# Performance work log

Hardware: AMD Instinct MI355X
Metric: run time of the kernel (lower is better)

Reference implementation:

```python
import jax, jax.numpy as jnp
import numpy as np

T, N, D, E, O = 2, 4096, 1024, 8, 1024

def setup_inputs() -> dict:
    key = jax.random.key(0)
    k1, k2, k3 = jax.random.split(key, 3)
    x = jax.random.normal(k1, (T, N, D), dtype=jnp.float32)
    Wg = jax.random.normal(k2, (T, D, E), dtype=jnp.float32) * (1.0 / np.sqrt(D))
    We = jax.random.normal(k3, (E, D, O), dtype=jnp.float32) * (1.0 / np.sqrt(D))
    return {"x": x, "Wg": Wg, "We": We, "k": 2}


def reference(x, Wg, We, k):
    # Per-task gating logits: [T, N, E]
    logits = jnp.einsum('tnd,tde->tne', x, Wg)
    # Top-k mask per token (scatter 1.0 at top-k indices)
    _, topk_idx = jax.lax.top_k(logits, k)                      # [T, N, k]
    mask = jax.nn.one_hot(topk_idx, E, dtype=logits.dtype).sum(-2)  # [T, N, E]
    masked = mask * logits
    gates = masked / (masked.sum(-1, keepdims=True) + 1e-9)     # [T, N, E]
    # Dense expert outputs (each expert is Linear(D, O)): [T, N, E, O]
    eout = jnp.einsum('tnd,edo->tneo', x, We)
    # Weighted combine over selected experts
    out = jnp.einsum('tne,tneo->tno', gates, eout)              # [T, N, O]
    return out
```

## Files before the change

### kernel.cpp

```cpp
#include <hip/hip_runtime.h>
#include <hip/hip_bf16.h>
#include <stdint.h>

#define T_ 2
#define N_ 4096
#define D_ 1024
#define E_ 8
#define O_ 1024

#define BM 128
#define BN 128
#define BK 32

typedef __attribute__((ext_vector_type(8))) short short8;
typedef __attribute__((ext_vector_type(4))) float f32x4;

#define AS1 __attribute__((address_space(1)))
#define AS3 __attribute__((address_space(3)))

__device__ inline void gld16(const unsigned short* g, unsigned short* l) {
    __builtin_amdgcn_global_load_lds((const AS1 unsigned int*)g,
                                     (AS3 unsigned int*)l, 16, 0, 0);
}

__device__ inline unsigned short f2bf(float f) {
    union { float f; unsigned u; } v; v.f = f;
    unsigned r = v.u + 0x7fff + ((v.u >> 16) & 1);
    return (unsigned short)(r >> 16);
}

__global__ __launch_bounds__(256) void prep_kernel(
    const float* __restrict__ x, const float* __restrict__ Wg,
    const float* __restrict__ We,
    unsigned short* __restrict__ xb, unsigned short* __restrict__ Wbp,
    int* __restrict__ route, float2* __restrict__ gpair,
    float* __restrict__ out)
{
    __shared__ __align__(16) char smem[E_ * D_ * 4];
    int tid = threadIdx.x;

    if (blockIdx.x >= 2048) {
        float4 z = {0.f, 0.f, 0.f, 0.f};
        float4* dst = (float4*)out + (size_t)(blockIdx.x - 2048) * 1024;
#pragma unroll
        for (int k = 0; k < 4; ++k) dst[k * 256 + tid] = z;
        return;
    }

    if (blockIdx.x < 1024) {
        float (*WgT)[D_] = (float(*)[D_])smem;
        int wave = tid >> 6, lane = tid & 63;
        int token0 = blockIdx.x * 8;
        int t = token0 >> 12;
        const float* wgb = Wg + (size_t)t * D_ * E_;

#pragma unroll
        for (int r = 0; r < 8; ++r) {
            int f = r * 1024 + tid * 4;
            float4 v = *(const float4*)(wgb + f);
            WgT[f & 7][f >> 3]             = v.x;
            WgT[(f + 1) & 7][(f + 1) >> 3] = v.y;
            WgT[(f + 2) & 7][(f + 2) >> 3] = v.z;
            WgT[(f + 3) & 7][(f + 3) >> 3] = v.w;
        }
        __syncthreads();

#pragma unroll
        for (int tl = 0; tl < 2; ++tl) {
            int token = token0 + wave * 2 + tl;
            const float* xrow = x + (size_t)token * D_;

            float4 xv[4];
#pragma unroll
            for (int c = 0; c < 4; ++c)
                xv[c] = *(const float4*)(xrow + c * 256 + lane * 4);

            float acc[E_] = {0.f, 0.f, 0.f, 0.f, 0.f, 0.f, 0.f, 0.f};
#pragma unroll
            for (int c = 0; c < 4; ++c) {
                int d0 = c * 256 + lane * 4;
                unsigned lo = f2bf(xv[c].x) | ((unsigned)f2bf(xv[c].y) << 16);
                unsigned hi = f2bf(xv[c].z) | ((unsigned)f2bf(xv[c].w) << 16);
                *(uint2*)(&xb[(size_t)token * D_ + d0]) = make_uint2(lo, hi);
#pragma unroll
                for (int e = 0; e < E_; ++e) {
                    float4 w = *(const float4*)(&WgT[e][d0]);
                    acc[e] += xv[c].x * w.x + xv[c].y * w.y + xv[c].z * w.z + xv[c].w * w.w;
                }
            }
#pragma unroll
            for (int off = 1; off < 64; off <<= 1) {
#pragma unroll
                for (int e = 0; e < E_; ++e) acc[e] += __shfl_xor(acc[e], off, 64);
            }

            if (lane == 0) {
                float best = acc[0]; int bi = 0;
#pragma unroll
                for (int e = 1; e < E_; ++e) if (acc[e] > best) { best = acc[e]; bi = e; }
                float sec = -INFINITY; int si = 0;
#pragma unroll
                for (int e = 0; e < E_; ++e) if (e != bi && acc[e] > sec) { sec = acc[e]; si = e; }
                float s = best + sec + 1e-9f;
                route[token] = bi | (si << 8);
                gpair[token] = make_float2(best / s, sec / s);
            }
        }
    } else {
        unsigned short* P = (unsigned short*)smem;

        int b = blockIdx.x - 1024;
        int e  = b >> 7;
        int oy = (b & 127) >> 3;
        int dz = b & 7;
        int o0 = oy * 64, d0 = dz * 128;

#pragma unroll
        for (int r = 0; r < 32; ++r) {
            int lin = r * 256 + tid;
            int dd = lin >> 6, oo = lin & 63;
            P[oo * 136 + dd] = f2bf(We[((size_t)(e * D_ + d0 + dd)) * O_ + o0 + oo]);
        }
        __syncthreads();

#pragma unroll
        for (int w = 0; w < 4; ++w) {
            int ci   = w * 256 + tid;
            int lane = ci & 63;
            int c16  = (ci >> 6) & 3;
            int ks   = ci >> 8;
            int fr = lane & 15, q = lane >> 4;
            uint4 v = *(const uint4*)&P[(c16 * 16 + fr) * 136 + ks * 32 + q * 8];
            int ot  = oy >> 1;
            int cb  = (oy * 4 + c16) & 7;
            int ksa = dz * 4 + ks;
            size_t idx = ((((size_t)(e * 8 + ot) * 32 + ksa) * 8 + cb) * 64 + lane) * 8;
            *(uint4*)(Wbp + idx) = v;
        }
    }
}

__global__ __launch_bounds__(1024) void build_lists(
    const int* __restrict__ route, const float2* __restrict__ gpair,
    int* __restrict__ toklist, float* __restrict__ gatelist,
    int* __restrict__ counts)
{
    int g = blockIdx.x;
    int t = g >> 3, e = g & 7;
    int tid = threadIdx.x;
    int wave = tid >> 6, lane = tid & 63;

    __shared__ int waveSum[16];

    int4 r4 = *(const int4*)(route + t * N_ + tid * 4);
    int rr[4] = {r4.x, r4.y, r4.z, r4.w};
    int sel[4], slot[4], mycnt = 0;
#pragma unroll
    for (int j = 0; j < 4; ++j) {
        int e0 = rr[j] & 255, e1 = (rr[j] >> 8) & 255;
        sel[j]  = (e0 == e) || (e1 == e);
        slot[j] = (e0 == e) ? 0 : 1;
        mycnt  += sel[j];
    }
    int x = mycnt;
#pragma unroll
    for (int off = 1; off < 64; off <<= 1) {
        int y = __shfl_up(x, off, 64);
        if (lane >= off) x += y;
    }
    if (lane == 63) waveSum[wave] = x;
    __syncthreads();
    int woff = 0, total = 0;
#pragma unroll
    for (int w = 0; w < 16; ++w) {
        int s = waveSum[w];
        total += s;
        woff += (w < wave) ? s : 0;
    }
    int p = woff + x - mycnt;
#pragma unroll
    for (int j = 0; j < 4; ++j) {
        if (sel[j]) {
            int n = tid * 4 + j;
            toklist[g * N_ + p] = n | (slot[j] << 16);
            float2 gp = gpair[t * N_ + n];
            gatelist[g * N_ + p] = (slot[j] == 0) ? gp.x : gp.y;
            ++p;
        }
    }
    if (tid == 0) counts[g] = total;
}

__global__ __launch_bounds__(512, 4) void moe_gemm(
    const unsigned short* __restrict__ xb,
    const unsigned short* __restrict__ Wbp,
    const int* __restrict__ toklist, const float* __restrict__ gatelist,
    const int* __restrict__ counts, float* __restrict__ out)
{
    int lin = blockIdx.x;
    int mt  = lin >> 7;
    int u   = lin & 127;
    int xcd = u & 7;
    int v   = u >> 3;
    int g   = 2 * xcd + (v >> 3);
    int ot  = v & 7;
    int t   = g >> 3;

    int cnt = counts[g];
    int m0 = mt * BM;
    if (m0 >= cnt) return;

    __shared__ __align__(16) unsigned short As[2][BM * BK];
    __shared__ int   tokS[BM];
    __shared__ float gateS[BM];

    int tid = threadIdx.x;
    if (tid < BM) {
        int r = m0 + tid;
        tokS[tid]  = (r < cnt) ? toklist[g * N_ + r]  : -1;
        gateS[tid] = (r < cnt) ? gatelist[g * N_ + r] : 0.f;
    }
    __syncthreads();

    int wave = tid >> 6, lane = tid & 63;
    int lr = lane >> 2;
    int sg = (lane & 3) ^ ((lane >> 3) & 3);
    int ar = wave * 16 + lr;
    int tok = max(tokS[ar], 0) & 0xFFFF;
    const unsigned short* ag = xb + ((size_t)(t * N_ + tok)) * D_ + sg * 8;

    const unsigned short* wf =
        Wbp + ((size_t)((g & 7) * 8 + ot) * 32) * 4096;
    int cb0 = (wave >> 1) * 2;
    const unsigned short* bp0 = wf + cb0 * 512 + lane * 8;
    const unsigned short* bp1 = bp0 + 512;

    int fr = lane & 15, q = lane >> 4;
    int wm = (wave & 1) * 64;
    int wn = (wave >> 1) * 32;
    int fp = (q ^ ((fr >> 1) & 3)) * 8;

    f32x4 acc[4][2];
#pragma unroll
    for (int mi = 0; mi < 4; ++mi)
#pragma unroll
        for (int ni = 0; ni < 2; ++ni) acc[mi][ni] = (f32x4){0.f, 0.f, 0.f, 0.f};

    short8 bf0[2], bf1[2];

    gld16(ag, &As[0][wave * 512]);
    asm volatile("" ::: "memory");
    bf0[0] = *(const short8*)(bp0);
    bf0[1] = *(const short8*)(bp1);

#define KSTEP(CUR, NXT, BC, BNX, IT)                                           \
    {                                                                          \
        asm volatile("s_waitcnt vmcnt(2)" ::: "memory");     \
        __builtin_amdgcn_s_barrier();                                          \
        asm volatile("" ::: "memory");       \
        int kk = (IT) + 1;                                                     \
        if (kk < D_ / BK) {                                                    \
            gld16(ag + (size_t)kk * BK, &As[NXT][wave * 512]);                 \
            asm volatile("" ::: "memory");     \
            BNX[0] = *(const short8*)(bp0 + (size_t)kk * 4096);                \
            BNX[1] = *(const short8*)(bp1 + (size_t)kk * 4096);                \
        }                                                                      \
        short8 af[4];                                                          \
        _Pragma("unroll") for (int mi = 0; mi < 4; ++mi)                       \
            af[mi] = *(const short8*)(&As[CUR][(wm + mi * 16 + fr) * BK + fp]);\
        _Pragma("unroll") for (int mi = 0; mi < 4; ++mi) {                     \
            acc[mi][0] = __builtin_amdgcn_mfma_f32_16x16x32_bf16(              \
                af[mi], BC[0], acc[mi][0], 0, 0, 0);                           \
            acc[mi][1] = __builtin_amdgcn_mfma_f32_16x16x32_bf16(              \
                af[mi], BC[1], acc[mi][1], 0, 0, 0);                           \
        }                                                                      \
    }

    for (int it = 0; it < D_ / BK; it += 2) {
        KSTEP(0, 1, bf0, bf1, it)
        KSTEP(1, 0, bf1, bf0, it + 1)
    }
#undef KSTEP

    float* outb = out + (size_t)t * N_ * O_;
    int ncol = ot * 128 + wn + fr;
#pragma unroll
    for (int mi = 0; mi < 4; ++mi) {
#pragma unroll
        for (int r = 0; r < 4; ++r) {
            int ml = wm + mi * 16 + q * 4 + r;
            int ent = tokS[ml];
            if (ent >= 0) {
                int tokk = ent & 0xFFFF;
                float gate = gateS[ml];
                float* orow = outb + (size_t)tokk * O_ + ncol;
#pragma unroll
                for (int ni = 0; ni < 2; ++ni)
                    unsafeAtomicAdd(orow + ni * 16, gate * acc[mi][ni][r]);
            }
        }
    }
}

extern "C" void kernel_launch(void* const* d_in, const int* in_sizes, int n_in,
                              void* d_out, int out_size, void* d_ws, size_t ws_size,
                              hipStream_t stream)
{
    const float* x  = (const float*)d_in[0];
    const float* Wg = (const float*)d_in[1];
    const float* We = (const float*)d_in[2];
    float* out = (float*)d_out;

    char* ws = (char*)d_ws;
    unsigned short* xb   = (unsigned short*)(ws);
    unsigned short* Wbp  = (unsigned short*)(ws + 16777216);
    int*   toklist       = (int*)  (ws + 33554432);
    float* gatelist      = (float*)(ws + 33816576);
    int*   counts        = (int*)  (ws + 34078720);
    int*   route         = (int*)  (ws + 34078976);
    float2* gpair        = (float2*)(ws + 34111744);

    prep_kernel<<<4096, 256, 0, stream>>>(x, Wg, We, xb, Wbp, route, gpair, out);
    build_lists<<<T_ * E_, 1024, 0, stream>>>(route, gpair, toklist, gatelist, counts);
    moe_gemm<<<(N_ / BM) * 8 * (T_ * E_), 512, 0, stream>>>(
        xb, Wbp, toklist, gatelist, counts, out);
}
```

Measured before the change: 198.3 us.

## Replace atomic output accumulation with per-slot bf16 stores and a combine pass

Drops the zero-fill of the fp32 output and the float atomics. Each GEMM tile now stores its gated result as bf16 into one half of the fp32 output word, picked by the token's top-k slot, and a new combine kernel adds the two halves. The prep kernel also gives each gate block twice as many tokens and switches the weight repack to float4 loads over smaller tiles, and the GEMM tile order is permuted. This saves the memset and atomic traffic but adds a full read and write pass over the output and rounds each expert's contribution to bf16, which costs accuracy.

```diff
diff --git a/kernel.cpp b/kernel.cpp
--- a/kernel.cpp
+++ b/kernel.cpp
@@ -33,24 +33,15 @@
     const float* __restrict__ x, const float* __restrict__ Wg,
     const float* __restrict__ We,
     unsigned short* __restrict__ xb, unsigned short* __restrict__ Wbp,
-    int* __restrict__ route, float2* __restrict__ gpair,
-    float* __restrict__ out)
+    int* __restrict__ route, float2* __restrict__ gpair)
 {
     __shared__ __align__(16) char smem[E_ * D_ * 4];
     int tid = threadIdx.x;
 
-    if (blockIdx.x >= 2048) {
-        float4 z = {0.f, 0.f, 0.f, 0.f};
-        float4* dst = (float4*)out + (size_t)(blockIdx.x - 2048) * 1024;
-#pragma unroll
-        for (int k = 0; k < 4; ++k) dst[k * 256 + tid] = z;
-        return;
-    }
-
-    if (blockIdx.x < 1024) {
+    if (blockIdx.x < 512) {
         float (*WgT)[D_] = (float(*)[D_])smem;
         int wave = tid >> 6, lane = tid & 63;
-        int token0 = blockIdx.x * 8;
+        int token0 = blockIdx.x * 16;
         int t = token0 >> 12;
         const float* wgb = Wg + (size_t)t * D_ * E_;
 
@@ -66,8 +57,8 @@
         __syncthreads();
 
 #pragma unroll
-        for (int tl = 0; tl < 2; ++tl) {
-            int token = token0 + wave * 2 + tl;
+        for (int tl = 0; tl < 4; ++tl) {
+            int token = token0 + wave * 4 + tl;
             const float* xrow = x + (size_t)token * D_;
 
             float4 xv[4];
@@ -109,32 +100,35 @@
     } else {
         unsigned short* P = (unsigned short*)smem;
 
-        int b = blockIdx.x - 1024;
+        int b  = blockIdx.x - 512;
         int e  = b >> 7;
-        int oy = (b & 127) >> 3;
-        int dz = b & 7;
-        int o0 = oy * 64, d0 = dz * 128;
-
-#pragma unroll
-        for (int r = 0; r < 32; ++r) {
-            int lin = r * 256 + tid;
-            int dd = lin >> 6, oo = lin & 63;
-            P[oo * 136 + dd] = f2bf(We[((size_t)(e * D_ + d0 + dd)) * O_ + o0 + oo]);
+        int r7 = b & 127;
+        int dz = r7 >> 2;
+        int ob = r7 & 3;
+        int d0 = dz * 32, o0 = ob * 256;
+
+#pragma unroll
+        for (int it = 0; it < 8; ++it) {
+            int lin = it * 256 + tid;
+            int dd = lin >> 6, o4 = lin & 63;
+            float4 v = *(const float4*)(We + ((size_t)(e * D_ + d0 + dd)) * O_ + o0 + o4 * 4);
+            P[(o4 * 4 + 0) * 40 + dd] = f2bf(v.x);
+            P[(o4 * 4 + 1) * 40 + dd] = f2bf(v.y);
+            P[(o4 * 4 + 2) * 40 + dd] = f2bf(v.z);
+            P[(o4 * 4 + 3) * 40 + dd] = f2bf(v.w);
         }
         __syncthreads();
 
 #pragma unroll
-        for (int w = 0; w < 4; ++w) {
-            int ci   = w * 256 + tid;
+        for (int it = 0; it < 4; ++it) {
+            int ci   = it * 256 + tid;
+            int cbl  = ci >> 6;
             int lane = ci & 63;
-            int c16  = (ci >> 6) & 3;
-            int ks   = ci >> 8;
             int fr = lane & 15, q = lane >> 4;
-            uint4 v = *(const uint4*)&P[(c16 * 16 + fr) * 136 + ks * 32 + q * 8];
-            int ot  = oy >> 1;
-            int cb  = (oy * 4 + c16) & 7;
-            int ksa = dz * 4 + ks;
-            size_t idx = ((((size_t)(e * 8 + ot) * 32 + ksa) * 8 + cb) * 64 + lane) * 8;
+            uint4 v = *(const uint4*)&P[(cbl * 16 + fr) * 40 + q * 8];
+            int ot = ob * 2 + (cbl >> 3);
+            int cb = cbl & 7;
+            size_t idx = ((((size_t)(e * 8 + ot) * 32 + dz) * 8 + cb) * 64 + lane) * 8;
             *(uint4*)(Wbp + idx) = v;
         }
     }
@@ -198,7 +192,8 @@
     const int* __restrict__ counts, float* __restrict__ out)
 {
     int lin = blockIdx.x;
-    int mt  = lin >> 7;
+    int qm  = lin >> 7;
+    int mt  = (qm == 0) ? 8 : (qm <= 8 ? qm - 1 : qm);
     int u   = lin & 127;
     int xcd = u & 7;
     int v   = u >> 3;
@@ -292,14 +287,30 @@
             int ent = tokS[ml];
             if (ent >= 0) {
                 int tokk = ent & 0xFFFF;
+                int slot = ent >> 16;
                 float gate = gateS[ml];
-                float* orow = outb + (size_t)tokk * O_ + ncol;
-#pragma unroll
-                for (int ni = 0; ni < 2; ++ni)
-                    unsafeAtomicAdd(orow + ni * 16, gate * acc[mi][ni][r]);
+#pragma unroll
+                for (int ni = 0; ni < 2; ++ni) {
+                    unsigned short* p =
+                        (unsigned short*)(outb + (size_t)tokk * O_ + ncol + ni * 16);
+                    p[slot] = f2bf(gate * acc[mi][ni][r]);
+                }
             }
         }
     }
+}
+
+__global__ __launch_bounds__(256) void combine_kernel(float* __restrict__ out)
+{
+    size_t i = ((size_t)blockIdx.x * 256 + threadIdx.x) * 4;
+    unsigned* po = (unsigned*)out;
+    uint4 v = *(uint4*)(po + i);
+    float4 r;
+    union { unsigned u; float f; } a, b;
+#define CMB(comp, src) a.u = (src) << 16; b.u = (src) & 0xFFFF0000u; comp = a.f + b.f
+    CMB(r.x, v.x); CMB(r.y, v.y); CMB(r.z, v.z); CMB(r.w, v.w);
+#undef CMB
+    *(float4*)(out + i) = r;
 }
 
 extern "C" void kernel_launch(void* const* d_in, const int* in_sizes, int n_in,
@@ -320,8 +331,9 @@
     int*   route         = (int*)  (ws + 34078976);
     float2* gpair        = (float2*)(ws + 34111744);
 
-    prep_kernel<<<4096, 256, 0, stream>>>(x, Wg, We, xb, Wbp, route, gpair, out);
+    prep_kernel<<<1536, 256, 0, stream>>>(x, Wg, We, xb, Wbp, route, gpair);
     build_lists<<<T_ * E_, 1024, 0, stream>>>(route, gpair, toklist, gatelist, counts);
     moe_gemm<<<(N_ / BM) * 8 * (T_ * E_), 512, 0, stream>>>(
         xb, Wbp, toklist, gatelist, counts, out);
-}
+    combine_kernel<<<((size_t)T_ * N_ * O_) / (256 * 4), 256, 0, stream>>>(out);
+}
```

After: 179.0 us. 1.11x faster.
